# Kernel optimization log

Measured on AMD Instinct MI355X. Metric: run time of the kernel, lower is better.

Reference implementation:

```python
import jax, jax.numpy as jnp
import numpy as np

D = 1024

def setup_inputs() -> dict:
    key = jax.random.key(0)
    ks = jax.random.split(key, 12)
    B, N, d = 4, 4096, D
    init_std = 0.02 / np.sqrt(d)  # matches _init_weights for value_proj / o_proj
    inp = {
        "h": jax.random.normal(ks[0], (B, N, d), dtype=jnp.float32),
        # relation_encoder: Linear(d, d//2) -> GELU -> Linear(d//2, 1)  (weights stored [in, out])
        "W_re1": jax.random.normal(ks[1], (d, d // 2), dtype=jnp.float32) * 0.02,
        "b_re1": jnp.zeros((d // 2,), dtype=jnp.float32),
        "W_re2": jax.random.normal(ks[2], (d // 2, 1), dtype=jnp.float32) * 0.02,
        "b_re2": jnp.zeros((1,), dtype=jnp.float32),
        # value_proj: Linear(d, d, bias=False), init std = 0.02/sqrt(d)
        "W_v": jax.random.normal(ks[3], (d, d), dtype=jnp.float32) * init_std,
        # relation_transform: Linear(2d, d) -> GELU -> Linear(d, d)
        "W_rt1": jax.random.normal(ks[4], (2 * d, d), dtype=jnp.float32) * 0.02,
        "b_rt1": jnp.zeros((d,), dtype=jnp.float32),
        "W_rt2": jax.random.normal(ks[5], (d, d), dtype=jnp.float32) * 0.02,
        "b_rt2": jnp.zeros((d,), dtype=jnp.float32),
        # o_proj: Linear(d, d, bias=False), init std = 0.02/sqrt(d)
        "W_o": jax.random.normal(ks[6], (d, d), dtype=jnp.float32) * init_std,
    }
    return inp


def reference(h, W_re1, b_re1, W_re2, b_re2, W_v, W_rt1, b_rt1, W_rt2, b_rt2, W_o):
    B, N, d = h.shape
    # relation_encoder MLP -> scalar logit per token (torch GELU is exact erf form)
    hidden = jax.nn.gelu(jnp.einsum('bnd,dk->bnk', h, W_re1) + b_re1, approximate=False)
    relation_logits = (jnp.einsum('bnk,ko->bno', hidden, W_re2) + b_re2)[..., 0]  # [B, N]
    relation_strength = jax.nn.sigmoid(relation_logits)  # [B, N]
    # pointer targets: round(sigmoid * (N-1)) clamped (jnp.round == torch.round, half-to-even)
    relation_targets = jnp.clip(
        jnp.round(relation_strength * (N - 1)).astype(jnp.int32), 0, N - 1
    )  # [B, N]
    # per-token gather of target hidden state within each batch row
    target_features = jnp.take_along_axis(h, relation_targets[..., None], axis=1)  # [B, N, d]
    source_values = jnp.einsum('bnd,de->bne', h, W_v)
    target_values = jnp.einsum('bnd,de->bne', target_features, W_v)
    relation_input = jnp.concatenate([source_values, target_values], axis=-1)  # [B, N, 2d]
    relation_output = jax.nn.gelu(
        jnp.einsum('bnf,fe->bne', relation_input, W_rt1) + b_rt1, approximate=False
    )
    relation_output = jnp.einsum('bne,ef->bnf', relation_output, W_rt2) + b_rt2
    z = jnp.einsum('bnd,de->bne', relation_output, W_o)  # [B, N, d]
    return (z, relation_targets, relation_strength)
```

## Files before the change

### kernel.cpp

```cpp
#include <hip/hip_runtime.h>
#include <math.h>
#include <type_traits>

#define DMODEL 1024
#define NSEQ   4096
#define MTOT   16384

typedef unsigned short ushortT;
typedef __attribute__((ext_vector_type(8))) short short8;
typedef __attribute__((ext_vector_type(4))) float f32x4;

__device__ __forceinline__ float gelu_f(float x) {
    return 0.5f * x * (1.0f + erff(x * 0.70710678118654752440f));
}
__device__ __forceinline__ double gelu_d(double x) {
    return 0.5 * x * (1.0 + erf(x * 0.70710678118654752440));
}
__device__ __forceinline__ ushortT f2bf(float f) {
    unsigned u = __float_as_uint(f);
    u += 0x7FFFu + ((u >> 16) & 1u);
    return (ushortT)(u >> 16);
}
__device__ __forceinline__ float bf2f(ushortT b) {
    return __uint_as_float(((unsigned)b) << 16);
}
__device__ __forceinline__ void gload16(const void* g, void* l) {
    __builtin_amdgcn_global_load_lds(
        (const __attribute__((address_space(1))) unsigned*)g,
        (__attribute__((address_space(3))) unsigned*)l, 16, 0, 0);
}

enum { EPI_BF16 = 0, EPI_GELU_BIAS_BF16 = 1, EPI_BIAS_F32 = 2, EPI_TRANS_BF16 = 3,
       EPI_GELU_ADDQ_BF16 = 4 };

template<int EPI>
__global__ __launch_bounds__(256)
void mfma_gemm(const ushortT* __restrict__ A, const ushortT* __restrict__ Bt,
               const float* __restrict__ bias, void* __restrict__ Cv,
               int K, int lda, int ldb, int ldc,
               const int* __restrict__ gidx, const ushortT* __restrict__ Qg)
{
    __shared__ ushortT As[128 * 32];
    __shared__ ushortT Bs[128 * 32];
    const int tid  = threadIdx.x;
    const int lane = tid & 63;
    const int w    = tid >> 6;
    const int wr   = (w >> 1) * 64;
    const int wc   = (w & 1) * 64;
    const int m0   = blockIdx.y * 128;
    const int n0   = blockIdx.x * 128;

    const int lrow = lane >> 2;
    const int lk   = (lane & 3) * 8;

    f32x4 acc[4][4];
    #pragma unroll
    for (int i = 0; i < 4; i++)
        #pragma unroll
        for (int j = 0; j < 4; j++) acc[i][j] = (f32x4){0.f, 0.f, 0.f, 0.f};

    for (int kk = 0; kk < K; kk += 32) {
        #pragma unroll
        for (int i = 0; i < 2; i++) {
            const ushortT* ga = A + (size_t)(m0 + w * 32 + i * 16 + lrow) * lda + kk + lk;
            gload16(ga, &As[(w * 32 + i * 16) * 32]);
            const ushortT* gb = Bt + (size_t)(n0 + w * 32 + i * 16 + lrow) * ldb + kk + lk;
            gload16(gb, &Bs[(w * 32 + i * 16) * 32]);
        }
        __syncthreads();

        const int mi = lane & 15;
        const int ko = (lane >> 4) * 8;
        short8 a[4], b[4];
        #pragma unroll
        for (int i = 0; i < 4; i++)
            a[i] = *(const short8*)&As[(wr + i * 16 + mi) * 32 + ko];
        #pragma unroll
        for (int j = 0; j < 4; j++)
            b[j] = *(const short8*)&Bs[(wc + j * 16 + mi) * 32 + ko];
        #pragma unroll
        for (int i = 0; i < 4; i++)
            #pragma unroll
            for (int j = 0; j < 4; j++)
                acc[i][j] = __builtin_amdgcn_mfma_f32_16x16x32_bf16(a[i], b[j], acc[i][j], 0, 0, 0);
        __syncthreads();
    }

    const int cr = (lane >> 4) * 4;
    const int cc = lane & 15;
    #pragma unroll
    for (int i = 0; i < 4; i++) {
        #pragma unroll
        for (int j = 0; j < 4; j++) {
            const int gr = m0 + wr + i * 16 + cr;
            const int gc = n0 + wc + j * 16 + cc;
            #pragma unroll
            for (int r = 0; r < 4; r++) {
                float v = acc[i][j][r];
                if constexpr (EPI == EPI_GELU_BIAS_BF16) v = gelu_f(v + bias[gc]);
                if constexpr (EPI == EPI_GELU_ADDQ_BF16) {
                    const int trow = gidx[gr + r];
                    v = gelu_f(v + bias[gc] + bf2f(Qg[(size_t)trow * DMODEL + gc]));
                }
                if constexpr (EPI == EPI_BIAS_F32)       v = v + bias[gc];
                if constexpr (EPI == EPI_BF16 || EPI == EPI_GELU_BIAS_BF16 ||
                              EPI == EPI_GELU_ADDQ_BF16)
                    ((ushortT*)Cv)[(size_t)(gr + r) * ldc + gc] = f2bf(v);
                else if constexpr (EPI == EPI_BIAS_F32)
                    ((float*)Cv)[(size_t)(gr + r) * ldc + gc] = v;
                else
                    ((ushortT*)Cv)[(size_t)gc * ldc + (gr + r)] = f2bf(v);
            }
        }
    }
}

__global__ __launch_bounds__(256)
void wsplit_gemm(const ushortT* __restrict__ Ah, const ushortT* __restrict__ Al,
                 const ushortT* __restrict__ Bh, const ushortT* __restrict__ Bl,
                 ushortT* __restrict__ Ct, int K, int lda, int ldb, int ldc)
{
    __shared__ ushortT Ash[128 * 32], Asl[128 * 32];
    __shared__ ushortT Bsh[128 * 32], Bsl[128 * 32];
    const int tid  = threadIdx.x;
    const int lane = tid & 63;
    const int w    = tid >> 6;
    const int wr   = (w >> 1) * 64;
    const int wc   = (w & 1) * 64;
    const int m0   = blockIdx.y * 128;
    const int n0   = blockIdx.x * 128;
    const int lrow = lane >> 2;
    const int lk   = (lane & 3) * 8;

    f32x4 acc[4][4];
    #pragma unroll
    for (int i = 0; i < 4; i++)
        #pragma unroll
        for (int j = 0; j < 4; j++) acc[i][j] = (f32x4){0.f, 0.f, 0.f, 0.f};

    for (int kk = 0; kk < K; kk += 32) {
        #pragma unroll
        for (int i = 0; i < 2; i++) {
            const size_t aoff = (size_t)(m0 + w * 32 + i * 16 + lrow) * lda + kk + lk;
            const size_t boff = (size_t)(n0 + w * 32 + i * 16 + lrow) * ldb + kk + lk;
            const int ldst = (w * 32 + i * 16) * 32;
            gload16(Ah + aoff, &Ash[ldst]);
            gload16(Al + aoff, &Asl[ldst]);
            gload16(Bh + boff, &Bsh[ldst]);
            gload16(Bl + boff, &Bsl[ldst]);
        }
        __syncthreads();

        const int mi = lane & 15;
        const int ko = (lane >> 4) * 8;
        short8 ah[4], al[4], bh[4], bl[4];
        #pragma unroll
        for (int i = 0; i < 4; i++) {
            ah[i] = *(const short8*)&Ash[(wr + i * 16 + mi) * 32 + ko];
            al[i] = *(const short8*)&Asl[(wr + i * 16 + mi) * 32 + ko];
        }
        #pragma unroll
        for (int j = 0; j < 4; j++) {
            bh[j] = *(const short8*)&Bsh[(wc + j * 16 + mi) * 32 + ko];
            bl[j] = *(const short8*)&Bsl[(wc + j * 16 + mi) * 32 + ko];
        }
        #pragma unroll
        for (int i = 0; i < 4; i++)
            #pragma unroll
            for (int j = 0; j < 4; j++) {
                acc[i][j] = __builtin_amdgcn_mfma_f32_16x16x32_bf16(ah[i], bh[j], acc[i][j], 0, 0, 0);
                acc[i][j] = __builtin_amdgcn_mfma_f32_16x16x32_bf16(ah[i], bl[j], acc[i][j], 0, 0, 0);
                acc[i][j] = __builtin_amdgcn_mfma_f32_16x16x32_bf16(al[i], bh[j], acc[i][j], 0, 0, 0);
            }
        __syncthreads();
    }

    const int cr = (lane >> 4) * 4;
    const int cc = lane & 15;
    #pragma unroll
    for (int i = 0; i < 4; i++)
        #pragma unroll
        for (int j = 0; j < 4; j++) {
            const int gr = m0 + wr + i * 16 + cr;
            const int gc = n0 + wc + j * 16 + cc;
            #pragma unroll
            for (int r = 0; r < 4; r++)
                Ct[(size_t)gc * ldc + (gr + r)] = f2bf(acc[i][j][r]);
        }
}

__global__ __launch_bounds__(256)
void enc_gemm(const ushortT* __restrict__ Ah, const ushortT* __restrict__ Al,
              const ushortT* __restrict__ Bh, const ushortT* __restrict__ Bl,
              const float* __restrict__ bias, float* __restrict__ C)
{
    __shared__ ushortT Ash[128 * 32], Asl[128 * 32];
    __shared__ ushortT Bsh[128 * 32], Bsl[128 * 32];
    const int tid  = threadIdx.x;
    const int lane = tid & 63;
    const int w    = tid >> 6;
    const int wr   = (w >> 1) * 64;
    const int wc   = (w & 1) * 64;
    const int m0   = blockIdx.y * 128;
    const int n0   = blockIdx.x * 128;
    const int lrow = lane >> 2;
    const int lk   = (lane & 3) * 8;

    f32x4 acc[4][4];
    #pragma unroll
    for (int i = 0; i < 4; i++)
        #pragma unroll
        for (int j = 0; j < 4; j++) acc[i][j] = (f32x4){0.f, 0.f, 0.f, 0.f};

    for (int kk = 0; kk < DMODEL; kk += 32) {
        #pragma unroll
        for (int i = 0; i < 2; i++) {
            const size_t aoff = (size_t)(m0 + w * 32 + i * 16 + lrow) * DMODEL + kk + lk;
            const size_t boff = (size_t)(n0 + w * 32 + i * 16 + lrow) * DMODEL + kk + lk;
            const int ldst = (w * 32 + i * 16) * 32;
            gload16(Ah + aoff, &Ash[ldst]);
            gload16(Al + aoff, &Asl[ldst]);
            gload16(Bh + boff, &Bsh[ldst]);
            gload16(Bl + boff, &Bsl[ldst]);
        }
        __syncthreads();

        const int mi = lane & 15;
        const int ko = (lane >> 4) * 8;
        short8 ah[4], al[4], bh[4], bl[4];
        #pragma unroll
        for (int i = 0; i < 4; i++) {
            ah[i] = *(const short8*)&Ash[(wr + i * 16 + mi) * 32 + ko];
            al[i] = *(const short8*)&Asl[(wr + i * 16 + mi) * 32 + ko];
        }
        #pragma unroll
        for (int j = 0; j < 4; j++) {
            bh[j] = *(const short8*)&Bsh[(wc + j * 16 + mi) * 32 + ko];
            bl[j] = *(const short8*)&Bsl[(wc + j * 16 + mi) * 32 + ko];
        }
        #pragma unroll
        for (int i = 0; i < 4; i++)
            #pragma unroll
            for (int j = 0; j < 4; j++) {
                acc[i][j] = __builtin_amdgcn_mfma_f32_16x16x32_bf16(ah[i], bh[j], acc[i][j], 0, 0, 0);
                acc[i][j] = __builtin_amdgcn_mfma_f32_16x16x32_bf16(ah[i], bl[j], acc[i][j], 0, 0, 0);
                acc[i][j] = __builtin_amdgcn_mfma_f32_16x16x32_bf16(al[i], bh[j], acc[i][j], 0, 0, 0);
            }
        __syncthreads();
    }

    const int cr = (lane >> 4) * 4;
    const int cc = lane & 15;
    #pragma unroll
    for (int i = 0; i < 4; i++)
        #pragma unroll
        for (int j = 0; j < 4; j++) {
            const int gr = m0 + wr + i * 16 + cr;
            const int gc = n0 + wc + j * 16 + cc;
            #pragma unroll
            for (int r = 0; r < 4; r++)
                C[(size_t)(gr + r) * 512 + gc] = gelu_f(acc[i][j][r] + bias[gc]);
        }
}

__global__ __launch_bounds__(256)
void target2_k(const float* __restrict__ Genc, const float* __restrict__ W2,
               const float* __restrict__ b2, float* __restrict__ outT,
               float* __restrict__ outS, int* __restrict__ gidx,
               int* __restrict__ cnt, int* __restrict__ list)
{
    const int m = blockIdx.x * 4 + (threadIdx.x >> 6);
    const int lane = threadIdx.x & 63;
    const float* gr = Genc + (size_t)m * 512;
    double s = 0.0;
    #pragma unroll 4
    for (int j = lane; j < 512; j += 64) s = fma((double)gr[j], (double)W2[j], s);
    #pragma unroll
    for (int off = 32; off; off >>= 1) s += __shfl_down(s, off);
    if (lane == 0) {
        double logit = s + (double)b2[0];
        double str = 1.0 / (1.0 + exp(-logit));
        double r = str * (double)(NSEQ - 1);
        double n = rint(r);
        double dist = fabs(r - n);
        n = fmin(fmax(n, 0.0), (double)(NSEQ - 1));
        int t = (int)n;
        outT[m] = (float)t;
        outS[m] = (float)str;
        gidx[m] = ((m >> 12) << 12) + t;
        if (dist > 0.46) {
            int ix = atomicAdd(cnt, 1);
            list[ix] = m;
        }
    }
}

#define FIX_T 2
__global__ __launch_bounds__(256)
void fixup_k(const float* __restrict__ h, const float* __restrict__ W1,
             const float* __restrict__ b1, const float* __restrict__ W2,
             const float* __restrict__ b2, const int* __restrict__ cnt_p,
             const int* __restrict__ list, float* __restrict__ outT,
             float* __restrict__ outS, int* __restrict__ gidx)
{
    __shared__ float hrow[FIX_T][1024];
    __shared__ double red[4][FIX_T];
    const int tid = threadIdx.x;
    const int cnt = *cnt_p;
    for (int base = (int)blockIdx.x * FIX_T; base < cnt;
         base += (int)gridDim.x * FIX_T) {
        const int nt = min(FIX_T, cnt - base);
        for (int t = 0; t < nt; t++) {
            const int m = list[base + t];
            const float4* src = (const float4*)(h + (size_t)m * 1024);
            ((float4*)hrow[t])[tid] = src[tid];
        }
        __syncthreads();

        double a[FIX_T][2];
        #pragma unroll
        for (int t = 0; t < FIX_T; t++) { a[t][0] = 0.0; a[t][1] = 0.0; }

        #pragma unroll 4
        for (int k = 0; k < 1024; k++) {
            const double wa = (double)W1[(size_t)k * 512 + tid];
            const double wb = (double)W1[(size_t)k * 512 + tid + 256];
            #pragma unroll
            for (int t = 0; t < FIX_T; t++) {
                const double hv = (double)hrow[t][k];
                a[t][0] = fma(hv, wa, a[t][0]);
                a[t][1] = fma(hv, wb, a[t][1]);
            }
        }

        const double w2a = (double)W2[tid], w2b = (double)W2[tid + 256];
        const double b1a = (double)b1[tid], b1b = (double)b1[tid + 256];
        const int lane = tid & 63, w = tid >> 6;
        #pragma unroll
        for (int t = 0; t < FIX_T; t++) {
            double v = w2a * gelu_d(a[t][0] + b1a) + w2b * gelu_d(a[t][1] + b1b);
            #pragma unroll
            for (int off = 32; off; off >>= 1) v += __shfl_down(v, off);
            if (lane == 0) red[w][t] = v;
        }
        __syncthreads();
        if (tid < nt) {
            const int t = tid;
            double logit = red[0][t] + red[1][t] + red[2][t] + red[3][t] + (double)b2[0];
            double str = 1.0 / (1.0 + exp(-logit));
            double r = str * (double)(NSEQ - 1);
            double n = rint(r);
            n = fmin(fmax(n, 0.0), (double)(NSEQ - 1));
            const int m = list[base + t];
            const int ti = (int)n;
            outT[m] = (float)ti;
            outS[m] = (float)str;
            gidx[m] = ((m >> 12) << 12) + ti;
        }
        __syncthreads();
    }
}

__global__ __launch_bounds__(256)
void biascomb_k(const float* __restrict__ brt2, const float* __restrict__ Wo,
                float* __restrict__ bc)
{
    int j = blockIdx.x * 256 + threadIdx.x;
    float s = 0.f;
    for (int e = 0; e < DMODEL; e++) s = fmaf(brt2[e], Wo[e * DMODEL + j], s);
    bc[j] = s;
}

__global__ __launch_bounds__(256)
void cast_k(const float* __restrict__ x, ushortT* __restrict__ y, int n)
{
    int i = (blockIdx.x * 256 + threadIdx.x) * 4;
    if (i < n) {
        float4 v = *(const float4*)(x + i);
        ushortT o[4] = { f2bf(v.x), f2bf(v.y), f2bf(v.z), f2bf(v.w) };
        *(ulong1*)&y[i] = *(ulong1*)o;
    }
}

__global__ __launch_bounds__(256)
void split_cast_k(const float* __restrict__ x, ushortT* __restrict__ yh,
                  ushortT* __restrict__ yl, int n)
{
    int i = (blockIdx.x * 256 + threadIdx.x) * 4;
    if (i < n) {
        float4 v = *(const float4*)(x + i);
        float vv[4] = { v.x, v.y, v.z, v.w };
        ushortT oh[4], ol[4];
        #pragma unroll
        for (int q = 0; q < 4; q++) {
            oh[q] = f2bf(vv[q]);
            ol[q] = f2bf(vv[q] - bf2f(oh[q]));
        }
        *(ulong1*)&yh[i] = *(ulong1*)oh;
        *(ulong1*)&yl[i] = *(ulong1*)ol;
    }
}

__global__ __launch_bounds__(256)
void transcast_k(const float* __restrict__ W, ushortT* __restrict__ Wt, int K, int N)
{
    __shared__ float t[32][33];
    const int tx = threadIdx.x & 31, ty = threadIdx.x >> 5;
    const int n0 = blockIdx.x * 32, k0 = blockIdx.y * 32;
    #pragma unroll
    for (int r = 0; r < 32; r += 8)
        t[ty + r][tx] = W[(size_t)(k0 + ty + r) * N + n0 + tx];
    __syncthreads();
    #pragma unroll
    for (int r = 0; r < 32; r += 8)
        Wt[(size_t)(n0 + ty + r) * K + k0 + tx] = f2bf(t[tx][ty + r]);
}

__global__ __launch_bounds__(256)
void split_transcast_k(const float* __restrict__ W, ushortT* __restrict__ Wth,
                       ushortT* __restrict__ Wtl, int K, int N)
{
    __shared__ float t[32][33];
    const int tx = threadIdx.x & 31, ty = threadIdx.x >> 5;
    const int n0 = blockIdx.x * 32, k0 = blockIdx.y * 32;
    #pragma unroll
    for (int r = 0; r < 32; r += 8)
        t[ty + r][tx] = W[(size_t)(k0 + ty + r) * N + n0 + tx];
    __syncthreads();
    #pragma unroll
    for (int r = 0; r < 32; r += 8) {
        float x = t[tx][ty + r];
        ushortT hi = f2bf(x);
        Wth[(size_t)(n0 + ty + r) * K + k0 + tx] = hi;
        Wtl[(size_t)(n0 + ty + r) * K + k0 + tx] = f2bf(x - bf2f(hi));
    }
}

extern "C" void kernel_launch(void* const* d_in, const int* in_sizes, int n_in,
                              void* d_out, int out_size, void* d_ws, size_t ws_size,
                              hipStream_t stream)
{
    const float* h     = (const float*)d_in[0];
    const float* W_re1 = (const float*)d_in[1];
    const float* b_re1 = (const float*)d_in[2];
    const float* W_re2 = (const float*)d_in[3];
    const float* b_re2 = (const float*)d_in[4];
    const float* W_v   = (const float*)d_in[5];
    const float* W_rt1 = (const float*)d_in[6];
    const float* b_rt1 = (const float*)d_in[7];
    const float* W_rt2 = (const float*)d_in[8];
    const float* b_rt2 = (const float*)d_in[9];
    const float* W_o   = (const float*)d_in[10];

    float* z    = (float*)d_out;
    float* outT = z + (size_t)MTOT * DMODEL;
    float* outS = outT + MTOT;
    ushortT* Q    = (ushortT*)z;
    ushortT* h_hi = (ushortT*)z + (size_t)MTOT * DMODEL;

    char* ws = (char*)d_ws;
    ushortT* G       = (ushortT*)ws;
    float*   Genc    = (float*)(ws + (32ull  << 20));
    ushortT* h_lo    = (ushortT*)(ws + (64ull  << 20));
    ushortT* Wrt1t_h = (ushortT*)(ws + (96ull  << 20));
    ushortT* Wrt1t_l = (ushortT*)(ws + (100ull << 20));
    ushortT* Wv_h    = (ushortT*)(ws + (104ull << 20));
    ushortT* Wv_l    = (ushortT*)(ws + (106ull << 20));
    ushortT* Wa_t    = (ushortT*)(ws + (108ull << 20));
    ushortT* Wb_t    = (ushortT*)(ws + (110ull << 20));
    ushortT* Wo_t    = (ushortT*)(ws + (112ull << 20));
    ushortT* Wrt2_b  = (ushortT*)(ws + (114ull << 20));
    ushortT* Wc_t    = (ushortT*)(ws + (116ull << 20));
    ushortT* Wre1t_h = (ushortT*)(ws + (118ull << 20));
    ushortT* Wre1t_l = (ushortT*)(ws + (119ull << 20));
    float*   b_c     = (float*)(ws + (120ull << 20));
    int*     cnt     = (int*)  (ws + (120ull << 20) + 4096);
    int*     gidx    = (int*)  (ws + (120ull << 20) + 8192);
    int*     list    = (int*)  (ws + (120ull << 20) + 8192 + 65536);

    split_cast_k<<<dim3(MTOT * DMODEL / 1024), 256, 0, stream>>>(h, h_hi, h_lo, MTOT * DMODEL);
    split_cast_k<<<dim3(DMODEL * DMODEL / 1024), 256, 0, stream>>>(W_v, Wv_h, Wv_l, DMODEL * DMODEL);
    split_transcast_k<<<dim3(16, 32), 256, 0, stream>>>(W_re1, Wre1t_h, Wre1t_l, DMODEL, 512);
    split_transcast_k<<<dim3(32, 64), 256, 0, stream>>>(W_rt1, Wrt1t_h, Wrt1t_l, 2 * DMODEL, DMODEL);
    cast_k<<<dim3(DMODEL * DMODEL / 1024), 256, 0, stream>>>(W_rt2, Wrt2_b, DMODEL * DMODEL);
    transcast_k<<<dim3(32, 32), 256, 0, stream>>>(W_o, Wo_t, DMODEL, DMODEL);
    biascomb_k<<<dim3(4), 256, 0, stream>>>(b_rt2, W_o, b_c);

    wsplit_gemm<<<dim3(8, 8), 256, 0, stream>>>(Wv_h, Wv_l, Wrt1t_h, Wrt1t_l,
                                                Wa_t, DMODEL, DMODEL, 2 * DMODEL, DMODEL);
    wsplit_gemm<<<dim3(8, 8), 256, 0, stream>>>(Wv_h, Wv_l, Wrt1t_h + DMODEL, Wrt1t_l + DMODEL,
                                                Wb_t, DMODEL, DMODEL, 2 * DMODEL, DMODEL);

    enc_gemm<<<dim3(4, 128), 256, 0, stream>>>(h_hi, h_lo, Wre1t_h, Wre1t_l, b_re1, Genc);

    hipMemsetAsync(cnt, 0, 4, stream);
    target2_k<<<dim3(MTOT / 4), 256, 0, stream>>>(Genc, W_re2, b_re2, outT, outS, gidx, cnt, list);
    fixup_k<<<dim3(4096), 256, 0, stream>>>(h, W_re1, b_re1, W_re2, b_re2, cnt, list,
                                            outT, outS, gidx);

    mfma_gemm<EPI_TRANS_BF16><<<dim3(8, 8), 256, 0, stream>>>(
        Wrt2_b, Wo_t, nullptr, (void*)Wc_t, DMODEL, DMODEL, DMODEL, DMODEL, nullptr, nullptr);

    mfma_gemm<EPI_BF16><<<dim3(8, 128), 256, 0, stream>>>(
        h_hi, Wb_t, nullptr, (void*)Q, DMODEL, DMODEL, DMODEL, DMODEL, nullptr, nullptr);

    mfma_gemm<EPI_GELU_ADDQ_BF16><<<dim3(8, 128), 256, 0, stream>>>(
        h_hi, Wa_t, b_rt1, (void*)G, DMODEL, DMODEL, DMODEL, DMODEL, gidx, Q);

    mfma_gemm<EPI_BIAS_F32><<<dim3(8, 128), 256, 0, stream>>>(
        G, Wc_t, b_c, (void*)z, DMODEL, DMODEL, DMODEL, DMODEL, nullptr, nullptr);
}
```

Measured before the change: 703.0 us.

## Fuse P and Q GEMMs sharing A tile, add gather-GELU kernel and block swizzle

Merges the two h-by-weight GEMMs, one producing source values and one producing target values, into a single kernel. It loads each A tile once and accumulates into two accumulator sets. The gathered GELU that used to live in the GEMM epilogue becomes a separate elementwise kernel that reads an fp32 P buffer and a bf16 Q buffer. A grid swizzle is added to the GEMMs to improve L2 reuse, and the two weight-split GEMMs are merged into one launch. The cost is extra fp32 P traffic, one more launch, and higher register pressure from the doubled accumulators.

```diff
diff --git a/kernel.cpp b/kernel.cpp
--- a/kernel.cpp
+++ b/kernel.cpp
@@ -30,15 +30,13 @@
         (__attribute__((address_space(3))) unsigned*)l, 16, 0, 0);
 }
 
-enum { EPI_BF16 = 0, EPI_GELU_BIAS_BF16 = 1, EPI_BIAS_F32 = 2, EPI_TRANS_BF16 = 3,
-       EPI_GELU_ADDQ_BF16 = 4 };
+enum { EPI_BIAS_F32 = 2, EPI_TRANS_BF16 = 3 };
 
 template<int EPI>
 __global__ __launch_bounds__(256)
 void mfma_gemm(const ushortT* __restrict__ A, const ushortT* __restrict__ Bt,
                const float* __restrict__ bias, void* __restrict__ Cv,
-               int K, int lda, int ldb, int ldc,
-               const int* __restrict__ gidx, const ushortT* __restrict__ Qg)
+               int K, int lda, int ldb, int ldc, int cpx)
 {
     __shared__ ushortT As[128 * 32];
     __shared__ ushortT Bs[128 * 32];
@@ -47,8 +45,10 @@
     const int w    = tid >> 6;
     const int wr   = (w >> 1) * 64;
     const int wc   = (w & 1) * 64;
-    const int m0   = blockIdx.y * 128;
-    const int n0   = blockIdx.x * 128;
+    const int flat = blockIdx.x + (blockIdx.y << 3);
+    const int swz  = (flat & 7) * cpx + (flat >> 3);
+    const int n0   = (swz & 7) * 128;
+    const int m0   = (swz >> 3) * 128;
 
     const int lrow = lane >> 2;
     const int lk   = (lane & 3) * 8;
@@ -97,17 +97,8 @@
             #pragma unroll
             for (int r = 0; r < 4; r++) {
                 float v = acc[i][j][r];
-                if constexpr (EPI == EPI_GELU_BIAS_BF16) v = gelu_f(v + bias[gc]);
-                if constexpr (EPI == EPI_GELU_ADDQ_BF16) {
-                    const int trow = gidx[gr + r];
-                    v = gelu_f(v + bias[gc] + bf2f(Qg[(size_t)trow * DMODEL + gc]));
-                }
-                if constexpr (EPI == EPI_BIAS_F32)       v = v + bias[gc];
-                if constexpr (EPI == EPI_BF16 || EPI == EPI_GELU_BIAS_BF16 ||
-                              EPI == EPI_GELU_ADDQ_BF16)
-                    ((ushortT*)Cv)[(size_t)(gr + r) * ldc + gc] = f2bf(v);
-                else if constexpr (EPI == EPI_BIAS_F32)
-                    ((float*)Cv)[(size_t)(gr + r) * ldc + gc] = v;
+                if constexpr (EPI == EPI_BIAS_F32)
+                    ((float*)Cv)[(size_t)(gr + r) * ldc + gc] = v + bias[gc];
                 else
                     ((ushortT*)Cv)[(size_t)gc * ldc + (gr + r)] = f2bf(v);
             }
@@ -116,9 +107,103 @@
 }
 
 __global__ __launch_bounds__(256)
+void pq_gemm(const ushortT* __restrict__ A, const ushortT* __restrict__ Ba,
+             const ushortT* __restrict__ Bb, const float* __restrict__ bias,
+             float* __restrict__ P, ushortT* __restrict__ Q)
+{
+    __shared__ ushortT As[128 * 32];
+    __shared__ ushortT Bsa[128 * 32];
+    __shared__ ushortT Bsb[128 * 32];
+    const int tid  = threadIdx.x;
+    const int lane = tid & 63;
+    const int w    = tid >> 6;
+    const int wr   = (w >> 1) * 64;
+    const int wc   = (w & 1) * 64;
+    const int flat = blockIdx.x + (blockIdx.y << 3);
+    const int swz  = (flat & 7) * 128 + (flat >> 3);
+    const int n0   = (swz & 7) * 128;
+    const int m0   = (swz >> 3) * 128;
+
+    const int lrow = lane >> 2;
+    const int lk   = (lane & 3) * 8;
+
+    f32x4 acc_a[4][4], acc_b[4][4];
+    #pragma unroll
+    for (int i = 0; i < 4; i++)
+        #pragma unroll
+        for (int j = 0; j < 4; j++) {
+            acc_a[i][j] = (f32x4){0.f, 0.f, 0.f, 0.f};
+            acc_b[i][j] = (f32x4){0.f, 0.f, 0.f, 0.f};
+        }
+
+    for (int kk = 0; kk < DMODEL; kk += 32) {
+        #pragma unroll
+        for (int i = 0; i < 2; i++) {
+            const int row = w * 32 + i * 16;
+            gload16(A  + (size_t)(m0 + row + lrow) * DMODEL + kk + lk, &As[row * 32]);
+            gload16(Ba + (size_t)(n0 + row + lrow) * DMODEL + kk + lk, &Bsa[row * 32]);
+            gload16(Bb + (size_t)(n0 + row + lrow) * DMODEL + kk + lk, &Bsb[row * 32]);
+        }
+        __syncthreads();
+
+        const int mi = lane & 15;
+        const int ko = (lane >> 4) * 8;
+        short8 a[4];
+        #pragma unroll
+        for (int i = 0; i < 4; i++)
+            a[i] = *(const short8*)&As[(wr + i * 16 + mi) * 32 + ko];
+        #pragma unroll
+        for (int j = 0; j < 4; j++) {
+            short8 ba = *(const short8*)&Bsa[(wc + j * 16 + mi) * 32 + ko];
+            short8 bb = *(const short8*)&Bsb[(wc + j * 16 + mi) * 32 + ko];
+            #pragma unroll
+            for (int i = 0; i < 4; i++) {
+                acc_a[i][j] = __builtin_amdgcn_mfma_f32_16x16x32_bf16(a[i], ba, acc_a[i][j], 0, 0, 0);
+                acc_b[i][j] = __builtin_amdgcn_mfma_f32_16x16x32_bf16(a[i], bb, acc_b[i][j], 0, 0, 0);
+            }
+        }
+        __syncthreads();
+    }
+
+    const int cr = (lane >> 4) * 4;
+    const int cc = lane & 15;
+    #pragma unroll
+    for (int i = 0; i < 4; i++) {
+        #pragma unroll
+        for (int j = 0; j < 4; j++) {
+            const int gr = m0 + wr + i * 16 + cr;
+            const int gc = n0 + wc + j * 16 + cc;
+            #pragma unroll
+            for (int r = 0; r < 4; r++) {
+                P[(size_t)(gr + r) * DMODEL + gc] = acc_a[i][j][r] + bias[gc];
+                Q[(size_t)(gr + r) * DMODEL + gc] = f2bf(acc_b[i][j][r]);
+            }
+        }
+    }
+}
+
+__global__ __launch_bounds__(256)
+void gelu_gather_k(const float* __restrict__ P, const ushortT* __restrict__ Q,
+                   const int* __restrict__ gidx, ushortT* __restrict__ G)
+{
+    const int m = blockIdx.x;
+    int t = gidx[m];
+    t = max(0, min(t, MTOT - 1));
+    const int c = threadIdx.x * 4;
+    float4 p = *(const float4*)(P + (size_t)m * DMODEL + c);
+    ushort4 q = *(const ushort4*)(Q + (size_t)t * DMODEL + c);
+    ushortT o[4];
+    o[0] = f2bf(gelu_f(p.x + bf2f(q.x)));
+    o[1] = f2bf(gelu_f(p.y + bf2f(q.y)));
+    o[2] = f2bf(gelu_f(p.z + bf2f(q.z)));
+    o[3] = f2bf(gelu_f(p.w + bf2f(q.w)));
+    *(ulong1*)(G + (size_t)m * DMODEL + c) = *(ulong1*)o;
+}
+
+__global__ __launch_bounds__(256)
 void wsplit_gemm(const ushortT* __restrict__ Ah, const ushortT* __restrict__ Al,
-                 const ushortT* __restrict__ Bh, const ushortT* __restrict__ Bl,
-                 ushortT* __restrict__ Ct, int K, int lda, int ldb, int ldc)
+                 const ushortT* __restrict__ Bh0, const ushortT* __restrict__ Bl0,
+                 ushortT* __restrict__ Ct0, int K, int lda, int ldb, int ldc)
 {
     __shared__ ushortT Ash[128 * 32], Asl[128 * 32];
     __shared__ ushortT Bsh[128 * 32], Bsl[128 * 32];
@@ -127,8 +212,12 @@
     const int w    = tid >> 6;
     const int wr   = (w >> 1) * 64;
     const int wc   = (w & 1) * 64;
-    const int m0   = blockIdx.y * 128;
+    const int sel  = blockIdx.y >> 3;
+    const int m0   = (blockIdx.y & 7) * 128;
     const int n0   = blockIdx.x * 128;
+    const ushortT* Bh = Bh0 + sel * 1024;
+    const ushortT* Bl = Bl0 + sel * 1024;
+    ushortT* Ct = Ct0 + (size_t)sel * 1024 * 1024;
     const int lrow = lane >> 2;
     const int lk   = (lane & 3) * 8;
 
@@ -201,8 +290,10 @@
     const int w    = tid >> 6;
     const int wr   = (w >> 1) * 64;
     const int wc   = (w & 1) * 64;
-    const int m0   = blockIdx.y * 128;
-    const int n0   = blockIdx.x * 128;
+    const int flat = blockIdx.x + (blockIdx.y << 2);
+    const int swz  = (flat & 7) * 64 + (flat >> 3);
+    const int n0   = (swz & 3) * 128;
+    const int m0   = (swz >> 2) * 128;
     const int lrow = lane >> 2;
     const int lk   = (lane & 3) * 8;
 
@@ -289,13 +380,13 @@
         outS[m] = (float)str;
         gidx[m] = ((m >> 12) << 12) + t;
         if (dist > 0.46) {
-            int ix = atomicAdd(cnt, 1);
+            int ix = atomicAdd(cnt, 1) & (MTOT - 1);
             list[ix] = m;
         }
     }
 }
 
-#define FIX_T 2
+#define FIX_T 4
 __global__ __launch_bounds__(256)
 void fixup_k(const float* __restrict__ h, const float* __restrict__ W1,
              const float* __restrict__ b1, const float* __restrict__ W2,
@@ -306,7 +397,7 @@
     __shared__ float hrow[FIX_T][1024];
     __shared__ double red[4][FIX_T];
     const int tid = threadIdx.x;
-    const int cnt = *cnt_p;
+    const int cnt = min(*cnt_p, MTOT);
     for (int base = (int)blockIdx.x * FIX_T; base < cnt;
          base += (int)gridDim.x * FIX_T) {
         const int nt = min(FIX_T, cnt - base);
@@ -462,12 +553,12 @@
     ushortT* G       = (ushortT*)ws;
     float*   Genc    = (float*)(ws + (32ull  << 20));
     ushortT* h_lo    = (ushortT*)(ws + (64ull  << 20));
+    float*   P       = (float*)(ws + (32ull  << 20));
     ushortT* Wrt1t_h = (ushortT*)(ws + (96ull  << 20));
     ushortT* Wrt1t_l = (ushortT*)(ws + (100ull << 20));
     ushortT* Wv_h    = (ushortT*)(ws + (104ull << 20));
     ushortT* Wv_l    = (ushortT*)(ws + (106ull << 20));
     ushortT* Wa_t    = (ushortT*)(ws + (108ull << 20));
-    ushortT* Wb_t    = (ushortT*)(ws + (110ull << 20));
     ushortT* Wo_t    = (ushortT*)(ws + (112ull << 20));
     ushortT* Wrt2_b  = (ushortT*)(ws + (114ull << 20));
     ushortT* Wc_t    = (ushortT*)(ws + (116ull << 20));
@@ -477,6 +568,7 @@
     int*     cnt     = (int*)  (ws + (120ull << 20) + 4096);
     int*     gidx    = (int*)  (ws + (120ull << 20) + 8192);
     int*     list    = (int*)  (ws + (120ull << 20) + 8192 + 65536);
+    ushortT* Wb_t    = Wa_t + (size_t)1024 * 1024;
 
     split_cast_k<<<dim3(MTOT * DMODEL / 1024), 256, 0, stream>>>(h, h_hi, h_lo, MTOT * DMODEL);
     split_cast_k<<<dim3(DMODEL * DMODEL / 1024), 256, 0, stream>>>(W_v, Wv_h, Wv_l, DMODEL * DMODEL);
@@ -486,10 +578,8 @@
     transcast_k<<<dim3(32, 32), 256, 0, stream>>>(W_o, Wo_t, DMODEL, DMODEL);
     biascomb_k<<<dim3(4), 256, 0, stream>>>(b_rt2, W_o, b_c);
 
-    wsplit_gemm<<<dim3(8, 8), 256, 0, stream>>>(Wv_h, Wv_l, Wrt1t_h, Wrt1t_l,
-                                                Wa_t, DMODEL, DMODEL, 2 * DMODEL, DMODEL);
-    wsplit_gemm<<<dim3(8, 8), 256, 0, stream>>>(Wv_h, Wv_l, Wrt1t_h + DMODEL, Wrt1t_l + DMODEL,
-                                                Wb_t, DMODEL, DMODEL, 2 * DMODEL, DMODEL);
+    wsplit_gemm<<<dim3(8, 16), 256, 0, stream>>>(Wv_h, Wv_l, Wrt1t_h, Wrt1t_l,
+                                                 Wa_t, DMODEL, DMODEL, 2 * DMODEL, DMODEL);
 
     enc_gemm<<<dim3(4, 128), 256, 0, stream>>>(h_hi, h_lo, Wre1t_h, Wre1t_l, b_re1, Genc);
 
@@ -499,14 +589,12 @@
                                             outT, outS, gidx);
 
     mfma_gemm<EPI_TRANS_BF16><<<dim3(8, 8), 256, 0, stream>>>(
-        Wrt2_b, Wo_t, nullptr, (void*)Wc_t, DMODEL, DMODEL, DMODEL, DMODEL, nullptr, nullptr);
-
-    mfma_gemm<EPI_BF16><<<dim3(8, 128), 256, 0, stream>>>(
-        h_hi, Wb_t, nullptr, (void*)Q, DMODEL, DMODEL, DMODEL, DMODEL, nullptr, nullptr);
-
-    mfma_gemm<EPI_GELU_ADDQ_BF16><<<dim3(8, 128), 256, 0, stream>>>(
-        h_hi, Wa_t, b_rt1, (void*)G, DMODEL, DMODEL, DMODEL, DMODEL, gidx, Q);
+        Wrt2_b, Wo_t, nullptr, (void*)Wc_t, DMODEL, DMODEL, DMODEL, DMODEL, 8);
+
+    pq_gemm<<<dim3(8, 128), 256, 0, stream>>>(h_hi, Wa_t, Wb_t, b_rt1, P, Q);
+
+    gelu_gather_k<<<dim3(MTOT), 256, 0, stream>>>(P, Q, gidx, G);
 
     mfma_gemm<EPI_BIAS_F32><<<dim3(8, 128), 256, 0, stream>>>(
-        G, Wc_t, b_c, (void*)z, DMODEL, DMODEL, DMODEL, DMODEL, nullptr, nullptr);
-}
+        G, Wc_t, b_c, (void*)z, DMODEL, DMODEL, DMODEL, DMODEL, 128);
+}
```

Measured after the change: 666.1 us. 1.06x faster.

## Merge source/target GEMMs into one wide GEMM with a separate gelu-gather pass

Applied to the files above, without the earlier changes.

The two h-projections (against Wa and Wb) are merged into one GEMM with N=2048 that writes P (fp32 plus bias) and Q (bf16). A new elementwise kernel then gathers Q by target index, adds it to P and applies GELU, replacing the gather-in-epilogue GEMM. The two wsplit weight GEMMs are merged into one launch, and GEMM tiles are swizzled for L2 locality. This removes a launch and the scattered Q reads in the GEMM epilogue, at the cost of an extra fp32 P round-trip through memory.

```diff
diff --git a/kernel.cpp b/kernel.cpp
--- a/kernel.cpp
+++ b/kernel.cpp
@@ -30,15 +30,13 @@
         (__attribute__((address_space(3))) unsigned*)l, 16, 0, 0);
 }
 
-enum { EPI_BF16 = 0, EPI_GELU_BIAS_BF16 = 1, EPI_BIAS_F32 = 2, EPI_TRANS_BF16 = 3,
-       EPI_GELU_ADDQ_BF16 = 4 };
-
-template<int EPI>
+enum { EPI_BIAS_F32 = 2, EPI_TRANS_BF16 = 3, EPI_PQ = 5 };
+
+template<int EPI, int NXT>
 __global__ __launch_bounds__(256)
 void mfma_gemm(const ushortT* __restrict__ A, const ushortT* __restrict__ Bt,
                const float* __restrict__ bias, void* __restrict__ Cv,
-               int K, int lda, int ldb, int ldc,
-               const int* __restrict__ gidx, const ushortT* __restrict__ Qg)
+               void* __restrict__ Cv2, int K, int lda, int ldb, int ldc, int cpx)
 {
     __shared__ ushortT As[128 * 32];
     __shared__ ushortT Bs[128 * 32];
@@ -47,8 +45,10 @@
     const int w    = tid >> 6;
     const int wr   = (w >> 1) * 64;
     const int wc   = (w & 1) * 64;
-    const int m0   = blockIdx.y * 128;
-    const int n0   = blockIdx.x * 128;
+    const int flat = blockIdx.x + blockIdx.y * NXT;
+    const int swz  = (flat & 7) * cpx + (flat >> 3);
+    const int n0   = (swz & (NXT - 1)) * 128;
+    const int m0   = (swz / NXT) * 128;
 
     const int lrow = lane >> 2;
     const int lk   = (lane & 3) * 8;
@@ -97,28 +97,43 @@
             #pragma unroll
             for (int r = 0; r < 4; r++) {
                 float v = acc[i][j][r];
-                if constexpr (EPI == EPI_GELU_BIAS_BF16) v = gelu_f(v + bias[gc]);
-                if constexpr (EPI == EPI_GELU_ADDQ_BF16) {
-                    const int trow = gidx[gr + r];
-                    v = gelu_f(v + bias[gc] + bf2f(Qg[(size_t)trow * DMODEL + gc]));
+                if constexpr (EPI == EPI_BIAS_F32) {
+                    ((float*)Cv)[(size_t)(gr + r) * ldc + gc] = v + bias[gc];
+                } else if constexpr (EPI == EPI_PQ) {
+                    if (gc < 1024)
+                        ((float*)Cv)[(size_t)(gr + r) * ldc + gc] = v + bias[gc];
+                    else
+                        ((ushortT*)Cv2)[(size_t)(gr + r) * ldc + (gc - 1024)] = f2bf(v);
+                } else {
+                    ((ushortT*)Cv)[(size_t)gc * ldc + (gr + r)] = f2bf(v);
                 }
-                if constexpr (EPI == EPI_BIAS_F32)       v = v + bias[gc];
-                if constexpr (EPI == EPI_BF16 || EPI == EPI_GELU_BIAS_BF16 ||
-                              EPI == EPI_GELU_ADDQ_BF16)
-                    ((ushortT*)Cv)[(size_t)(gr + r) * ldc + gc] = f2bf(v);
-                else if constexpr (EPI == EPI_BIAS_F32)
-                    ((float*)Cv)[(size_t)(gr + r) * ldc + gc] = v;
-                else
-                    ((ushortT*)Cv)[(size_t)gc * ldc + (gr + r)] = f2bf(v);
             }
         }
     }
 }
 
 __global__ __launch_bounds__(256)
+void gelu_gather_k(const float* __restrict__ P, const ushortT* __restrict__ Q,
+                   const int* __restrict__ gidx, ushortT* __restrict__ G)
+{
+    const int m = blockIdx.x;
+    int t = gidx[m];
+    t = max(0, min(t, MTOT - 1));
+    const int c = threadIdx.x * 4;
+    float4 p = *(const float4*)(P + (size_t)m * DMODEL + c);
+    ushort4 q = *(const ushort4*)(Q + (size_t)t * DMODEL + c);
+    ushortT o[4];
+    o[0] = f2bf(gelu_f(p.x + bf2f(q.x)));
+    o[1] = f2bf(gelu_f(p.y + bf2f(q.y)));
+    o[2] = f2bf(gelu_f(p.z + bf2f(q.z)));
+    o[3] = f2bf(gelu_f(p.w + bf2f(q.w)));
+    *(ulong1*)(G + (size_t)m * DMODEL + c) = *(ulong1*)o;
+}
+
+__global__ __launch_bounds__(256)
 void wsplit_gemm(const ushortT* __restrict__ Ah, const ushortT* __restrict__ Al,
-                 const ushortT* __restrict__ Bh, const ushortT* __restrict__ Bl,
-                 ushortT* __restrict__ Ct, int K, int lda, int ldb, int ldc)
+                 const ushortT* __restrict__ Bh0, const ushortT* __restrict__ Bl0,
+                 ushortT* __restrict__ Ct0, int K, int lda, int ldb, int ldc)
 {
     __shared__ ushortT Ash[128 * 32], Asl[128 * 32];
     __shared__ ushortT Bsh[128 * 32], Bsl[128 * 32];
@@ -127,8 +142,12 @@
     const int w    = tid >> 6;
     const int wr   = (w >> 1) * 64;
     const int wc   = (w & 1) * 64;
-    const int m0   = blockIdx.y * 128;
+    const int sel  = blockIdx.y >> 3;
+    const int m0   = (blockIdx.y & 7) * 128;
     const int n0   = blockIdx.x * 128;
+    const ushortT* Bh = Bh0 + sel * 1024;
+    const ushortT* Bl = Bl0 + sel * 1024;
+    ushortT* Ct = Ct0 + (size_t)sel * 1024 * 1024;
     const int lrow = lane >> 2;
     const int lk   = (lane & 3) * 8;
 
@@ -201,8 +220,10 @@
     const int w    = tid >> 6;
     const int wr   = (w >> 1) * 64;
     const int wc   = (w & 1) * 64;
-    const int m0   = blockIdx.y * 128;
-    const int n0   = blockIdx.x * 128;
+    const int flat = blockIdx.x + (blockIdx.y << 2);
+    const int swz  = (flat & 7) * 64 + (flat >> 3);
+    const int n0   = (swz & 3) * 128;
+    const int m0   = (swz >> 2) * 128;
     const int lrow = lane >> 2;
     const int lk   = (lane & 3) * 8;
 
@@ -289,13 +310,13 @@
         outS[m] = (float)str;
         gidx[m] = ((m >> 12) << 12) + t;
         if (dist > 0.46) {
-            int ix = atomicAdd(cnt, 1);
+            int ix = atomicAdd(cnt, 1) & (MTOT - 1);
             list[ix] = m;
         }
     }
 }
 
-#define FIX_T 2
+#define FIX_T 4
 __global__ __launch_bounds__(256)
 void fixup_k(const float* __restrict__ h, const float* __restrict__ W1,
              const float* __restrict__ b1, const float* __restrict__ W2,
@@ -306,7 +327,7 @@
     __shared__ float hrow[FIX_T][1024];
     __shared__ double red[4][FIX_T];
     const int tid = threadIdx.x;
-    const int cnt = *cnt_p;
+    const int cnt = min(*cnt_p, MTOT);
     for (int base = (int)blockIdx.x * FIX_T; base < cnt;
          base += (int)gridDim.x * FIX_T) {
         const int nt = min(FIX_T, cnt - base);
@@ -462,12 +483,12 @@
     ushortT* G       = (ushortT*)ws;
     float*   Genc    = (float*)(ws + (32ull  << 20));
     ushortT* h_lo    = (ushortT*)(ws + (64ull  << 20));
+    float*   P       = (float*)(ws + (32ull  << 20));
     ushortT* Wrt1t_h = (ushortT*)(ws + (96ull  << 20));
     ushortT* Wrt1t_l = (ushortT*)(ws + (100ull << 20));
     ushortT* Wv_h    = (ushortT*)(ws + (104ull << 20));
     ushortT* Wv_l    = (ushortT*)(ws + (106ull << 20));
     ushortT* Wa_t    = (ushortT*)(ws + (108ull << 20));
-    ushortT* Wb_t    = (ushortT*)(ws + (110ull << 20));
     ushortT* Wo_t    = (ushortT*)(ws + (112ull << 20));
     ushortT* Wrt2_b  = (ushortT*)(ws + (114ull << 20));
     ushortT* Wc_t    = (ushortT*)(ws + (116ull << 20));
@@ -486,10 +507,8 @@
     transcast_k<<<dim3(32, 32), 256, 0, stream>>>(W_o, Wo_t, DMODEL, DMODEL);
     biascomb_k<<<dim3(4), 256, 0, stream>>>(b_rt2, W_o, b_c);
 
-    wsplit_gemm<<<dim3(8, 8), 256, 0, stream>>>(Wv_h, Wv_l, Wrt1t_h, Wrt1t_l,
-                                                Wa_t, DMODEL, DMODEL, 2 * DMODEL, DMODEL);
-    wsplit_gemm<<<dim3(8, 8), 256, 0, stream>>>(Wv_h, Wv_l, Wrt1t_h + DMODEL, Wrt1t_l + DMODEL,
-                                                Wb_t, DMODEL, DMODEL, 2 * DMODEL, DMODEL);
+    wsplit_gemm<<<dim3(8, 16), 256, 0, stream>>>(Wv_h, Wv_l, Wrt1t_h, Wrt1t_l,
+                                                 Wa_t, DMODEL, DMODEL, 2 * DMODEL, DMODEL);
 
     enc_gemm<<<dim3(4, 128), 256, 0, stream>>>(h_hi, h_lo, Wre1t_h, Wre1t_l, b_re1, Genc);
 
@@ -498,15 +517,14 @@
     fixup_k<<<dim3(4096), 256, 0, stream>>>(h, W_re1, b_re1, W_re2, b_re2, cnt, list,
                                             outT, outS, gidx);
 
-    mfma_gemm<EPI_TRANS_BF16><<<dim3(8, 8), 256, 0, stream>>>(
-        Wrt2_b, Wo_t, nullptr, (void*)Wc_t, DMODEL, DMODEL, DMODEL, DMODEL, nullptr, nullptr);
-
-    mfma_gemm<EPI_BF16><<<dim3(8, 128), 256, 0, stream>>>(
-        h_hi, Wb_t, nullptr, (void*)Q, DMODEL, DMODEL, DMODEL, DMODEL, nullptr, nullptr);
-
-    mfma_gemm<EPI_GELU_ADDQ_BF16><<<dim3(8, 128), 256, 0, stream>>>(
-        h_hi, Wa_t, b_rt1, (void*)G, DMODEL, DMODEL, DMODEL, DMODEL, gidx, Q);
-
-    mfma_gemm<EPI_BIAS_F32><<<dim3(8, 128), 256, 0, stream>>>(
-        G, Wc_t, b_c, (void*)z, DMODEL, DMODEL, DMODEL, DMODEL, nullptr, nullptr);
-}
+    mfma_gemm<EPI_TRANS_BF16, 8><<<dim3(8, 8), 256, 0, stream>>>(
+        Wrt2_b, Wo_t, nullptr, (void*)Wc_t, nullptr, DMODEL, DMODEL, DMODEL, DMODEL, 8);
+
+    mfma_gemm<EPI_PQ, 16><<<dim3(16, 128), 256, 0, stream>>>(
+        h_hi, Wa_t, b_rt1, (void*)P, (void*)Q, DMODEL, DMODEL, DMODEL, DMODEL, 256);
+
+    gelu_gather_k<<<dim3(MTOT), 256, 0, stream>>>(P, Q, gidx, G);
+
+    mfma_gemm<EPI_BIAS_F32, 8><<<dim3(8, 128), 256, 0, stream>>>(
+        G, Wc_t, b_c, (void*)z, nullptr, DMODEL, DMODEL, DMODEL, DMODEL, 128);
+}
```

New measurement: 645.0 us. 8.3% less time.
